# Kernel tuning notes

Measured on AMD Instinct MI355X. Metric: run time of the kernel, lower is better.

The kernel has to match this reference:

```python
import jax, jax.numpy as jnp
import numpy as np

N, T, DM = 8192, 32, 128   # nodes, patches, d_model (d_in = T*DM = 4096)
M, NNZ = 1024, 131072      # hyperedges, incidences
EPS = 1e-5
SLOPE = 0.2


def _bn(x, g, b, axes):
    # BatchNorm with batch statistics (training-mode math, eval dropout)
    m = jnp.mean(x, axis=axes, keepdims=True)
    v = jnp.var(x, axis=axes, keepdims=True)
    return (x - m) / jnp.sqrt(v + EPS) * g + b


def _hconv(x, he_attr, he_n, he_e, W, att, bias, heads):
    # PyG HypergraphConv, use_attention=True, attention_mode='node', concat=False
    out = W.shape[1] // heads
    xt = (x @ W).reshape(N, heads, out)          # [N, H, F]
    et = (he_attr @ W).reshape(M, heads, out)    # [M, H, F]
    xi = xt[he_n]                                # [nnz, H, F] gather node feats
    ej = et[he_e]                                # [nnz, H, F] gather edge feats
    alpha = jnp.sum(jnp.concatenate([xi, ej], axis=-1) * att, axis=-1)  # [nnz, H]
    alpha = jax.nn.leaky_relu(alpha, SLOPE)
    # segment softmax grouped by hyperedge (attention_mode='node')
    amax = jax.ops.segment_max(alpha, he_e, num_segments=M)
    ex = jnp.exp(alpha - amax[he_e])
    alpha = ex / jax.ops.segment_sum(ex, he_e, num_segments=M)[he_e]
    # degree normalizers (hyperedge_weight == 1)
    ones = jnp.ones((NNZ,), x.dtype)
    Dn = jax.ops.segment_sum(ones, he_n, num_segments=N)
    Dinv = jnp.where(Dn > 0, 1.0 / Dn, 0.0)
    Bm = jax.ops.segment_sum(ones, he_e, num_segments=M)
    Binv = jnp.where(Bm > 0, 1.0 / Bm, 0.0)
    # node -> edge, then edge -> node message passing
    eo = jax.ops.segment_sum(alpha[:, :, None] * Binv[he_e][:, None, None] * xi,
                             he_e, num_segments=M)                     # [M, H, F]
    no = jax.ops.segment_sum(alpha[:, :, None] * Dinv[he_n][:, None, None] * eo[he_e],
                             he_n, num_segments=N)                     # [N, H, F]
    return no.mean(axis=1) + bias  # concat=False -> mean over heads


def setup_inputs() -> dict:
    key = jax.random.key(0)
    ks = jax.random.split(key, 16)
    d_in = T * DM
    s = 0.02
    inp = {
        "x": jax.random.normal(ks[0], (N, T, DM), jnp.float32),
        "he_nodes": jax.random.randint(ks[1], (NNZ,), 0, N),
        "he_edges": jax.random.randint(ks[2], (NNZ,), 0, M),
        "W1": jax.random.normal(ks[3], (d_in, DM), jnp.float32) * s,
        "b1": jnp.zeros((DM,), jnp.float32),
        "g1": jnp.ones((DM,), jnp.float32), "be1": jnp.zeros((DM,), jnp.float32),
        "Wh1": jax.random.normal(ks[4], (DM, 4 * DM), jnp.float32) * s,
        "att1": jax.random.normal(ks[5], (1, 4, 2 * DM), jnp.float32) * s,
        "bh1": jnp.zeros((DM,), jnp.float32),
        "g2": jnp.ones((DM,), jnp.float32), "be2": jnp.zeros((DM,), jnp.float32),
        "Wh2": jax.random.normal(ks[6], (DM, DM), jnp.float32) * s,
        "att2": jax.random.normal(ks[7], (1, 1, 2 * DM), jnp.float32) * s,
        "bh2": jnp.zeros((DM,), jnp.float32),
        "g3": jnp.ones((DM,), jnp.float32), "be3": jnp.zeros((DM,), jnp.float32),
        "W3": jax.random.normal(ks[8], (DM, d_in), jnp.float32) * s,
        "b3": jnp.zeros((d_in,), jnp.float32),
        "g4": jnp.ones((DM,), jnp.float32), "be4": jnp.zeros((DM,), jnp.float32),
    }
    return inp


def reference(x, he_nodes, he_edges, W1, b1, g1, be1, Wh1, att1, bh1,
              g2, be2, Wh2, att2, bh2, g3, be3, W3, b3, g4, be4):
    src = x
    h = x.reshape(N, T * DM)
    h = jax.nn.leaky_relu(h @ W1 + b1, SLOPE)
    h = _bn(h, g1, be1, 0)
    # hyperedge_attr = incidence^T @ h  (== to_dense_adj(...).T @ h)
    he_attr = jax.ops.segment_sum(h[he_nodes], he_edges, num_segments=M)
    h = h + _hconv(h, he_attr, he_nodes, he_edges, Wh1, att1, bh1, 4)
    h = _bn(h, g2, be2, 0)
    he_attr = jax.ops.segment_sum(h[he_nodes], he_edges, num_segments=M)
    h = h + _hconv(h, he_attr, he_nodes, he_edges, Wh2, att2, bh2, 1)
    h = _bn(h, g3, be3, 0)
    h = jax.nn.leaky_relu(h @ W3 + b3, SLOPE)
    h = src + h.reshape(N, T, DM)
    h = _bn(h, g4, be4, (0, 1))  # BN over channel DM, stats over (N, T)
    return h
```

## Files before the change

kernel.cpp:

```cpp
#include <hip/hip_runtime.h>
#include <hip/hip_bf16.h>
#include <math.h>

#define NN   8192
#define TT   32
#define DIN  4096
#define MME  1024
#define NNZK 131072
#define EPSV 1e-5f
#define MALL (NN + MME)

typedef __attribute__((ext_vector_type(8))) short bf16x8;
typedef __attribute__((ext_vector_type(4))) float f32x4;

__device__ __forceinline__ float lrelu(float v){ return v > 0.f ? v : 0.2f*v; }
__device__ __forceinline__ short f2b(float f){
    union { __hip_bfloat16 h; short s; } u; u.h = __float2bfloat16(f); return u.s;
}
__device__ __forceinline__ float b2f(short s){
    union { float f; unsigned u; } u; u.u = ((unsigned)(unsigned short)s) << 16; return u.f;
}

__global__ void zero_i(int* p, int n){ int i = blockIdx.x*256 + threadIdx.x; if (i < n) p[i] = 0; }
__global__ void zero_f(float* p, int n){ int i = blockIdx.x*256 + threadIdx.x; if (i < n) p[i] = 0.f; }
__global__ void copy_i(const int* a, int* b, int n){ int i = blockIdx.x*256 + threadIdx.x; if (i < n) b[i] = a[i]; }

__global__ void count_seg(const int* __restrict__ he_n, const int* __restrict__ he_e,
                          int* __restrict__ ncnt, int* __restrict__ ecnt){
    int k = blockIdx.x*256 + threadIdx.x;
    if (k < NNZK){ atomicAdd(&ecnt[he_e[k]], 1); atomicAdd(&ncnt[he_n[k]], 1); }
}

__global__ void scan_excl(const int* __restrict__ cnt, int* __restrict__ off, int n){
    int t = threadIdx.x;
    int lane = t & 63, wv = t >> 6;
    int chunk = n >> 10;
    int base = t*chunk;
    int s = 0;
#pragma unroll 4
    for (int i = 0; i < chunk; i++) s += cnt[base+i];
    int v = s;
    for (int d = 1; d < 64; d <<= 1){
        int u = __shfl_up(v, d);
        if (lane >= d) v += u;
    }
    __shared__ int wsum[16];
    if (lane == 63) wsum[wv] = v;
    __syncthreads();
    if (wv == 0 && lane < 16){
        int w2 = wsum[lane];
        for (int d = 1; d < 16; d <<= 1){
            int u = __shfl_up(w2, d);
            if (lane >= d) w2 += u;
        }
        wsum[lane] = w2;
    }
    __syncthreads();
    int excl = v - s + (wv > 0 ? wsum[wv-1] : 0);
    for (int i = 0; i < chunk; i++){
        off[base+i] = excl;
        excl += cnt[base+i];
    }
    if (t == 1023) off[n] = excl;
}

__global__ void fill_perm(const int* __restrict__ seg, int* __restrict__ cur, int* __restrict__ perm){
    int k = blockIdx.x*256 + threadIdx.x;
    if (k < NNZK){ int p = atomicAdd(&cur[seg[k]], 1); perm[p] = k; }
}

__global__ __launch_bounds__(256) void convert_x(const float4* __restrict__ x,
                                                 bf16x8* __restrict__ xb, int n8){
    int stride = gridDim.x*256;
    for (int i = blockIdx.x*256 + threadIdx.x; i < n8; i += stride){
        float4 lo = x[2*i], hi = x[2*i+1];
        bf16x8 v;
        v[0]=f2b(lo.x); v[1]=f2b(lo.y); v[2]=f2b(lo.z); v[3]=f2b(lo.w);
        v[4]=f2b(hi.x); v[5]=f2b(hi.y); v[6]=f2b(hi.z); v[7]=f2b(hi.w);
        xb[i] = v;
    }
}

__global__ void wconv_t(const float* __restrict__ W, __hip_bfloat16* __restrict__ BT, int K, int N){
    __shared__ float tile[32][33];
    int k0 = blockIdx.y*32, n0 = blockIdx.x*32;
    int tx = threadIdx.x & 31, ty = threadIdx.x >> 5;
    for (int i = ty; i < 32; i += 8) tile[i][tx] = W[(size_t)(k0+i)*N + n0+tx];
    __syncthreads();
    for (int i = ty; i < 32; i += 8)
        BT[(size_t)(n0+i)*K + k0 + tx] = __float2bfloat16(tile[tx][i]);
}

#define SWZ(b) ((b) ^ ((((b) >> 6) & 7) << 4))

__global__ __launch_bounds__(256) void gemm_bb(
    const __hip_bfloat16* __restrict__ Ab, const __hip_bfloat16* __restrict__ Bwt,
    __hip_bfloat16* __restrict__ Cb, int M, int N, int K, int kchunk)
{
    __shared__ f32x4 WsRaw[512];
    __shared__ f32x4 XsRaw[512];
    char* Ws = (char*)WsRaw;
    char* Xs = (char*)XsRaw;
    const int tid = threadIdx.x;
    const int lane = tid & 63;
    const int w = tid >> 6;
    const int m0 = blockIdx.y << 7, n0 = blockIdx.x << 7;
    const int kz = blockIdx.z * kchunk;
    const int wN = (w >> 1) << 6, wM = (w & 1) << 6;

    const int s0 = tid, s1 = tid + 256;
    const int r0 = s0 >> 2, k0b = (s0 & 3) << 3;
    const int r1 = s1 >> 2, k1b = (s1 & 3) << 3;
    const __hip_bfloat16* pA0 = Ab + (size_t)(m0 + r0)*K + kz + k0b;
    const __hip_bfloat16* pA1 = Ab + (size_t)(m0 + r1)*K + kz + k1b;
    const __hip_bfloat16* pW0 = Bwt + (size_t)(n0 + r0)*K + kz + k0b;
    const __hip_bfloat16* pW1 = Bwt + (size_t)(n0 + r1)*K + kz + k1b;
    const int wo0 = SWZ(s0 << 4), wo1 = SWZ(s1 << 4);

    int rwOff[4], rxOff[4];
#pragma unroll
    for (int f = 0; f < 4; f++){
        rwOff[f] = SWZ((wN + f*16 + (lane & 15))*64 + ((lane >> 4) << 4));
        rxOff[f] = SWZ((wM + f*16 + (lane & 15))*64 + ((lane >> 4) << 4));
    }

    f32x4 acc[4][4] = {};

    bf16x8 a0 = *(const bf16x8*)pA0, a1 = *(const bf16x8*)pA1;
    bf16x8 w0 = *(const bf16x8*)pW0, w1 = *(const bf16x8*)pW1;

    const int nsteps = kchunk >> 5;
    for (int ks = 0; ks < nsteps; ks++){
        __syncthreads();
        *(bf16x8*)(Xs + wo0) = a0;
        *(bf16x8*)(Xs + wo1) = a1;
        *(bf16x8*)(Ws + wo0) = w0;
        *(bf16x8*)(Ws + wo1) = w1;
        __syncthreads();
        if (ks + 1 < nsteps){
            pA0 += 32; pA1 += 32; pW0 += 32; pW1 += 32;
            a0 = *(const bf16x8*)pA0; a1 = *(const bf16x8*)pA1;
            w0 = *(const bf16x8*)pW0; w1 = *(const bf16x8*)pW1;
        }
        bf16x8 wf[4], xf[4];
#pragma unroll
        for (int f = 0; f < 4; f++){
            wf[f] = *(const bf16x8*)(Ws + rwOff[f]);
            xf[f] = *(const bf16x8*)(Xs + rxOff[f]);
        }
#pragma unroll
        for (int i = 0; i < 4; i++)
#pragma unroll
            for (int j = 0; j < 4; j++)
                acc[i][j] = __builtin_amdgcn_mfma_f32_16x16x32_bf16(wf[i], xf[j], acc[i][j], 0, 0, 0);
    }

    const int mc = wM + (lane & 15);
    const int ncb = wN + ((lane >> 4) << 2);
    __hip_bfloat16* Cz = Cb + (size_t)blockIdx.z * ((size_t)M * (size_t)N);
#pragma unroll
    for (int j = 0; j < 4; j++){
        int row = m0 + mc + j*16;
#pragma unroll
        for (int i = 0; i < 4; i++){
            int col = n0 + ncb + i*16;
            f32x4 v = acc[i][j];
            short4 sv = { f2b(v[0]), f2b(v[1]), f2b(v[2]), f2b(v[3]) };
            *(short4*)&Cz[(size_t)row*N + col] = sv;
        }
    }
}

template<int MODE>
__global__ __launch_bounds__(256) void gemm_nt(
    const float* __restrict__ Aact, const __hip_bfloat16* __restrict__ Bwt,
    float* __restrict__ C, __hip_bfloat16* __restrict__ Cb, const float* __restrict__ bias,
    int M, int N, int K, int kchunk)
{
    __shared__ f32x4 WsRaw[512];
    __shared__ f32x4 XsRaw[512];
    char* Ws = (char*)WsRaw;
    char* Xs = (char*)XsRaw;
    const int tid = threadIdx.x;
    const int lane = tid & 63;
    const int w = tid >> 6;
    const int m0 = blockIdx.y << 7, n0 = blockIdx.x << 7;
    const int wN = (w >> 1) << 6, wM = (w & 1) << 6;

    const int s0 = tid, s1 = tid + 256;
    const int r0 = s0 >> 2, k0b = (s0 & 3) << 3;
    const int r1 = s1 >> 2, k1b = (s1 & 3) << 3;
    const float* pX0 = Aact + (size_t)(m0 + r0)*K + k0b;
    const float* pX1 = Aact + (size_t)(m0 + r1)*K + k1b;
    const __hip_bfloat16* pW0 = Bwt + (size_t)(n0 + r0)*K + k0b;
    const __hip_bfloat16* pW1 = Bwt + (size_t)(n0 + r1)*K + k1b;
    const int wo0 = SWZ(s0 << 4), wo1 = SWZ(s1 << 4);

    int rwOff[4], rxOff[4];
#pragma unroll
    for (int f = 0; f < 4; f++){
        rwOff[f] = SWZ((wN + f*16 + (lane & 15))*64 + ((lane >> 4) << 4));
        rxOff[f] = SWZ((wM + f*16 + (lane & 15))*64 + ((lane >> 4) << 4));
    }

    f32x4 acc[4][4] = {};

    float4 x0l = *(const float4*)pX0, x0h = *(const float4*)(pX0+4);
    float4 x1l = *(const float4*)pX1, x1h = *(const float4*)(pX1+4);
    bf16x8 w0 = *(const bf16x8*)pW0, w1 = *(const bf16x8*)pW1;

    const int nsteps = kchunk >> 5;
    for (int ks = 0; ks < nsteps; ks++){
        bf16x8 vx0, vx1;
        vx0[0]=f2b(x0l.x); vx0[1]=f2b(x0l.y); vx0[2]=f2b(x0l.z); vx0[3]=f2b(x0l.w);
        vx0[4]=f2b(x0h.x); vx0[5]=f2b(x0h.y); vx0[6]=f2b(x0h.z); vx0[7]=f2b(x0h.w);
        vx1[0]=f2b(x1l.x); vx1[1]=f2b(x1l.y); vx1[2]=f2b(x1l.z); vx1[3]=f2b(x1l.w);
        vx1[4]=f2b(x1h.x); vx1[5]=f2b(x1h.y); vx1[6]=f2b(x1h.z); vx1[7]=f2b(x1h.w);
        __syncthreads();
        *(bf16x8*)(Xs + wo0) = vx0;
        *(bf16x8*)(Xs + wo1) = vx1;
        *(bf16x8*)(Ws + wo0) = w0;
        *(bf16x8*)(Ws + wo1) = w1;
        __syncthreads();
        if (ks + 1 < nsteps){
            pX0 += 32; pX1 += 32; pW0 += 32; pW1 += 32;
            x0l = *(const float4*)pX0; x0h = *(const float4*)(pX0+4);
            x1l = *(const float4*)pX1; x1h = *(const float4*)(pX1+4);
            w0 = *(const bf16x8*)pW0;  w1 = *(const bf16x8*)pW1;
        }
        bf16x8 wf[4], xf[4];
#pragma unroll
        for (int f = 0; f < 4; f++){
            wf[f] = *(const bf16x8*)(Ws + rwOff[f]);
            xf[f] = *(const bf16x8*)(Xs + rxOff[f]);
        }
#pragma unroll
        for (int i = 0; i < 4; i++)
#pragma unroll
            for (int j = 0; j < 4; j++)
                acc[i][j] = __builtin_amdgcn_mfma_f32_16x16x32_bf16(wf[i], xf[j], acc[i][j], 0, 0, 0);
    }

    const int mc = wM + (lane & 15);
    const int ncb = wN + ((lane >> 4) << 2);
#pragma unroll
    for (int j = 0; j < 4; j++){
        int row = m0 + mc + j*16;
#pragma unroll
        for (int i = 0; i < 4; i++){
            int col = n0 + ncb + i*16;
            f32x4 v = acc[i][j];
            if (MODE == 0){
                *(float4*)&C[(size_t)row*N + col] = *(float4*)&v;
            } else if (MODE == 5){
                short4 sv = { f2b(v[0]), f2b(v[1]), f2b(v[2]), f2b(v[3]) };
                *(short4*)&Cb[(size_t)row*N + col] = sv;
            } else {
                float4 b4 = *(const float4*)&bias[col];
                short4 sv = { f2b(lrelu(v[0] + b4.x)), f2b(lrelu(v[1] + b4.y)),
                              f2b(lrelu(v[2] + b4.z)), f2b(lrelu(v[3] + b4.w)) };
                *(short4*)&Cb[(size_t)row*N + col] = sv;
            }
        }
    }
}

__global__ void reduce8s(const __hip_bfloat16* __restrict__ part, const float* __restrict__ bias,
                         float* __restrict__ out, int nf4, int parts, float* __restrict__ slots){
    int tid = threadIdx.x;
    int i = blockIdx.x*256 + tid;
    const short4* p4 = (const short4*)part;
    short4 v0 = p4[i];
    float4 s = { b2f(v0.x), b2f(v0.y), b2f(v0.z), b2f(v0.w) };
    for (int z = 1; z < parts; z++){
        short4 p = p4[(size_t)z*nf4 + i];
        s.x += b2f(p.x); s.y += b2f(p.y); s.z += b2f(p.z); s.w += b2f(p.w);
    }
    int c0 = (i & 31) << 2;
    s.x = lrelu(s.x + bias[c0+0]); s.y = lrelu(s.y + bias[c0+1]);
    s.z = lrelu(s.z + bias[c0+2]); s.w = lrelu(s.w + bias[c0+3]);
    ((float4*)out)[i] = s;
    __shared__ float S[128], Q[128];
    if (tid < 128){ S[tid] = 0.f; Q[tid] = 0.f; }
    __syncthreads();
    atomicAdd(&S[c0+0], s.x); atomicAdd(&Q[c0+0], s.x*s.x);
    atomicAdd(&S[c0+1], s.y); atomicAdd(&Q[c0+1], s.y*s.y);
    atomicAdd(&S[c0+2], s.z); atomicAdd(&Q[c0+2], s.z*s.z);
    atomicAdd(&S[c0+3], s.w); atomicAdd(&Q[c0+3], s.w*s.w);
    __syncthreads();
    if (tid < 128){
        int slot = blockIdx.x & 31;
        atomicAdd(&slots[slot*256 + tid], S[tid]);
        atomicAdd(&slots[slot*256 + 128 + tid], Q[tid]);
    }
}

__global__ __launch_bounds__(256) void final_stats(
    const bf16x8* __restrict__ xb, const bf16x8* __restrict__ f,
    float* __restrict__ slots, int n8)
{
    int tid = threadIdx.x;
    float s[8] = {0,0,0,0,0,0,0,0}, q[8] = {0,0,0,0,0,0,0,0};
    int stride = gridDim.x*256;
    for (int i = blockIdx.x*256 + tid; i < n8; i += stride){
        bf16x8 xv = xb[i], fv = f[i];
#pragma unroll
        for (int j = 0; j < 8; j++){
            float y = b2f(xv[j]) + b2f(fv[j]);
            s[j] += y; q[j] += y*y;
        }
    }
    __shared__ float S[128], Q[128];
    if (tid < 128){ S[tid] = 0.f; Q[tid] = 0.f; }
    __syncthreads();
    int c0 = (tid & 15) << 3;
#pragma unroll
    for (int j = 0; j < 8; j++){
        atomicAdd(&S[c0+j], s[j]);
        atomicAdd(&Q[c0+j], q[j]);
    }
    __syncthreads();
    if (tid < 128){
        int slot = blockIdx.x & 31;
        atomicAdd(&slots[slot*256 + tid], S[tid]);
        atomicAdd(&slots[slot*256 + 128 + tid], Q[tid]);
    }
}

__global__ __launch_bounds__(256) void final_apply(
    const bf16x8* __restrict__ xb, const bf16x8* __restrict__ f,
    const float* __restrict__ coef, float4* __restrict__ out, int n8)
{
    int tid = threadIdx.x;
    int c0 = (tid & 15) << 3;
    float sc[8], sh[8];
#pragma unroll
    for (int j = 0; j < 8; j++){ sc[j] = coef[c0+j]; sh[j] = coef[128+c0+j]; }
    int stride = gridDim.x*256;
    for (int i = blockIdx.x*256 + tid; i < n8; i += stride){
        bf16x8 xv = xb[i], fv = f[i];
        float4 lo, hi;
        lo.x = (b2f(xv[0]) + b2f(fv[0]))*sc[0] + sh[0];
        lo.y = (b2f(xv[1]) + b2f(fv[1]))*sc[1] + sh[1];
        lo.z = (b2f(xv[2]) + b2f(fv[2]))*sc[2] + sh[2];
        lo.w = (b2f(xv[3]) + b2f(fv[3]))*sc[3] + sh[3];
        hi.x = (b2f(xv[4]) + b2f(fv[4]))*sc[4] + sh[4];
        hi.y = (b2f(xv[5]) + b2f(fv[5]))*sc[5] + sh[5];
        hi.z = (b2f(xv[6]) + b2f(fv[6]))*sc[6] + sh[6];
        hi.w = (b2f(xv[7]) + b2f(fv[7]))*sc[7] + sh[7];
        out[2*i]   = lo;
        out[2*i+1] = hi;
    }
}

__global__ void bn_stats_v2(const float* __restrict__ x, float* __restrict__ slots, int rows){
    int cg = threadIdx.x & 31, rg = threadIdx.x >> 5;
    float4 s = {0,0,0,0}, q = {0,0,0,0};
    for (int r = blockIdx.x*8 + rg; r < rows; r += gridDim.x*8){
        float4 v = ((const float4*)x)[(size_t)r*32 + cg];
        s.x += v.x; q.x += v.x*v.x;
        s.y += v.y; q.y += v.y*v.y;
        s.z += v.z; q.z += v.z*v.z;
        s.w += v.w; q.w += v.w*v.w;
    }
    __shared__ float S[128], Q[128];
    if (threadIdx.x < 128){ S[threadIdx.x] = 0.f; Q[threadIdx.x] = 0.f; }
    __syncthreads();
    int c0 = cg << 2;
    atomicAdd(&S[c0+0], s.x); atomicAdd(&Q[c0+0], q.x);
    atomicAdd(&S[c0+1], s.y); atomicAdd(&Q[c0+1], q.y);
    atomicAdd(&S[c0+2], s.z); atomicAdd(&Q[c0+2], q.z);
    atomicAdd(&S[c0+3], s.w); atomicAdd(&Q[c0+3], q.w);
    __syncthreads();
    if (threadIdx.x < 128){
        int slot = blockIdx.x & 31;
        atomicAdd(&slots[slot*256 + threadIdx.x], S[threadIdx.x]);
        atomicAdd(&slots[slot*256 + 128 + threadIdx.x], Q[threadIdx.x]);
    }
}

__global__ void bn_finalize2(const float* __restrict__ slots, int nslots,
                             const float* __restrict__ g, const float* __restrict__ b,
                             float invR, float* __restrict__ coef){
    int c = threadIdx.x;
    float s = 0.f, q = 0.f;
    for (int k = 0; k < nslots; k++){ s += slots[k*256 + c]; q += slots[k*256 + 128 + c]; }
    float m = s*invR;
    float v = q*invR - m*m;
    float sc = g[c]*rsqrtf(v + EPSV);
    coef[c] = sc;
    coef[128 + c] = b[c] - m*sc;
}

__global__ void bn_apply4(float4* __restrict__ x, const float* __restrict__ coef, size_t n4){
    size_t i = (size_t)blockIdx.x*blockDim.x + threadIdx.x;
    size_t stride = (size_t)gridDim.x*blockDim.x;
    for (; i < n4; i += stride){
        int c0 = (int)(i & 31) * 4;
        float4 v = x[i];
        v.x = v.x*coef[c0+0] + coef[128+c0+0];
        v.y = v.y*coef[c0+1] + coef[128+c0+1];
        v.z = v.z*coef[c0+2] + coef[128+c0+2];
        v.w = v.w*coef[c0+3] + coef[128+c0+3];
        x[i] = v;
    }
}

__global__ void seg_sum_edge(const int* __restrict__ eoff, const int* __restrict__ eperm,
                             const int* __restrict__ he_n, const float* __restrict__ h,
                             float* __restrict__ out){
    int m = blockIdx.x, c = threadIdx.x;
    int s0 = eoff[m], cnt = eoff[m+1] - s0;
    __shared__ int sn[128];
    float acc = 0.f;
    for (int base = 0; base < cnt; base += 128){
        int i = base + c;
        if (i < cnt) sn[c] = he_n[eperm[s0+i]];
        __syncthreads();
        int lim = min(128, cnt - base);
        for (int j = 0; j < lim; j++) acc += h[(size_t)sn[j]*128 + c];
        __syncthreads();
    }
    out[(size_t)m*128 + c] = acc;
}

__global__ void row_att4b(const __hip_bfloat16* __restrict__ xt, const float* __restrict__ att,
                          int aoff, float* __restrict__ out){
    int n = blockIdx.x, lane = threadIdx.x;
#pragma unroll
    for (int h = 0; h < 4; h++){
        const __hip_bfloat16* xr = xt + (size_t)n*512 + h*128;
        const float* ar = att + h*256 + aoff;
        float s = b2f(((const short*)xr)[2*lane])*ar[2*lane]
                + b2f(((const short*)xr)[2*lane+1])*ar[2*lane+1];
        for (int d = 32; d > 0; d >>= 1) s += __shfl_down(s, d);
        if (lane == 0) out[n*4 + h] = s;
    }
}

template<int H>
__global__ void row_att(const float* __restrict__ xt, const float* __restrict__ att,
                        int aoff, float* __restrict__ out){
    int n = blockIdx.x, lane = threadIdx.x;
#pragma unroll
    for (int h = 0; h < H; h++){
        const float* xr = xt + (size_t)n*(H*128) + h*128;
        const float* ar = att + h*256 + aoff;
        float s = xr[lane]*ar[lane] + xr[lane+64]*ar[lane+64];
        for (int d = 32; d > 0; d >>= 1) s += __shfl_down(s, d);
        if (lane == 0) out[n*H + h] = s;
    }
}

template<int H>
__global__ void seg_softmax(const int* __restrict__ eoff, const int* __restrict__ eperm,
                            const int* __restrict__ he_n,
                            const float* __restrict__ ax, const float* __restrict__ ae,
                            float* __restrict__ alpha){
    int m = blockIdx.x, t = threadIdx.x;
    int s0 = eoff[m], cnt = eoff[m+1] - s0;
    if (cnt == 0) return;
    __shared__ float red[128];
    float aeh[H];
#pragma unroll
    for (int h = 0; h < H; h++) aeh[h] = ae[m*H + h];
    float lmax[H];
#pragma unroll
    for (int h = 0; h < H; h++) lmax[h] = -1e30f;
    for (int i = t; i < cnt; i += 128){
        int k = eperm[s0+i]; int n = he_n[k];
#pragma unroll
        for (int h = 0; h < H; h++){
            float v = lrelu(ax[n*H + h] + aeh[h]);
            alpha[(size_t)k*H + h] = v;
            lmax[h] = fmaxf(lmax[h], v);
        }
    }
    float gmax[H];
#pragma unroll
    for (int h = 0; h < H; h++){
        red[t] = lmax[h]; __syncthreads();
        for (int s = 64; s > 0; s >>= 1){ if (t < s) red[t] = fmaxf(red[t], red[t+s]); __syncthreads(); }
        gmax[h] = red[0]; __syncthreads();
    }
    float lsum[H];
#pragma unroll
    for (int h = 0; h < H; h++) lsum[h] = 0.f;
    for (int i = t; i < cnt; i += 128){
        int k = eperm[s0+i];
#pragma unroll
        for (int h = 0; h < H; h++){
            float ex = __expf(alpha[(size_t)k*H + h] - gmax[h]);
            alpha[(size_t)k*H + h] = ex;
            lsum[h] += ex;
        }
    }
    float ginv[H];
#pragma unroll
    for (int h = 0; h < H; h++){
        red[t] = lsum[h]; __syncthreads();
        for (int s = 64; s > 0; s >>= 1){ if (t < s) red[t] += red[t+s]; __syncthreads(); }
        ginv[h] = 1.f/red[0]; __syncthreads();
    }
    for (int i = t; i < cnt; i += 128){
        int k = eperm[s0+i];
#pragma unroll
        for (int h = 0; h < H; h++) alpha[(size_t)k*H + h] *= ginv[h];
    }
}

__global__ void seg_eo4(const int* __restrict__ eoff, const int* __restrict__ eperm,
                        const int* __restrict__ he_n,
                        const float* __restrict__ alpha, const __hip_bfloat16* __restrict__ xt,
                        float* __restrict__ eo){
    int m = blockIdx.x;
    int c = threadIdx.x & 127, hb = threadIdx.x >> 7;
    int s0 = eoff[m], cnt = eoff[m+1] - s0;
    __shared__ int sn[128];
    __shared__ float sa[128][4];
    float acc0 = 0.f, acc1 = 0.f;
    for (int base = 0; base < cnt; base += 128){
        int i = base + threadIdx.x;
        if (threadIdx.x < 128 && i < cnt){
            int k = eperm[s0+i];
            sn[threadIdx.x] = he_n[k];
#pragma unroll
            for (int h = 0; h < 4; h++) sa[threadIdx.x][h] = alpha[(size_t)k*4 + h];
        }
        __syncthreads();
        int lim = min(128, cnt - base);
        for (int j = 0; j < lim; j++){
            const short* xr = (const short*)(xt + (size_t)sn[j]*512);
            acc0 += sa[j][hb]   * b2f(xr[hb*128 + c]);
            acc1 += sa[j][hb+2] * b2f(xr[(hb+2)*128 + c]);
        }
        __syncthreads();
    }
    float binv = cnt > 0 ? 1.f/(float)cnt : 0.f;
    eo[(size_t)m*512 + hb*128 + c]     = acc0*binv;
    eo[(size_t)m*512 + (hb+2)*128 + c] = acc1*binv;
}

__global__ void seg_eo1(const int* __restrict__ eoff, const int* __restrict__ eperm,
                        const int* __restrict__ he_n,
                        const float* __restrict__ alpha, const float* __restrict__ xt,
                        float* __restrict__ eo){
    int m = blockIdx.x, c = threadIdx.x;
    int s0 = eoff[m], cnt = eoff[m+1] - s0;
    __shared__ int sn[128];
    __shared__ float sa[128];
    float acc = 0.f;
    for (int base = 0; base < cnt; base += 128){
        int i = base + c;
        if (i < cnt){
            int k = eperm[s0+i];
            sn[c] = he_n[k];
            sa[c] = alpha[k];
        }
        __syncthreads();
        int lim = min(128, cnt - base);
        for (int j = 0; j < lim; j++) acc += sa[j]*xt[(size_t)sn[j]*128 + c];
        __syncthreads();
    }
    float binv = cnt > 0 ? 1.f/(float)cnt : 0.f;
    eo[(size_t)m*128 + c] = acc*binv;
}

template<int H>
__global__ void seg_node_out(const int* __restrict__ noff, const int* __restrict__ nperm,
                             const int* __restrict__ he_e,
                             const float* __restrict__ alpha, const float* __restrict__ eo,
                             const float* __restrict__ hin, const float* __restrict__ bias,
                             float* __restrict__ hout){
    int n = blockIdx.x, c = threadIdx.x;
    int s0 = noff[n], cnt = noff[n+1] - s0;
    float acc = 0.f;
    for (int i = 0; i < cnt; i++){
        int k = nperm[s0+i]; int e = he_e[k];
        const float* er = eo + (size_t)e*(128*H);
#pragma unroll
        for (int h = 0; h < H; h++) acc += alpha[(size_t)k*H + h]*er[h*128 + c];
    }
    float dinv = cnt > 0 ? 1.f/((float)cnt*(float)H) : 0.f;
    hout[(size_t)n*128 + c] = hin[(size_t)n*128 + c] + bias[c] + acc*dinv;
}

extern "C" void kernel_launch(void* const* d_in, const int* in_sizes, int n_in,
                              void* d_out, int out_size, void* d_ws, size_t ws_size,
                              hipStream_t stream){
    const float* x    = (const float*)d_in[0];
    const int*   he_n = (const int*)  d_in[1];
    const int*   he_e = (const int*)  d_in[2];
    const float* W1   = (const float*)d_in[3];
    const float* b1   = (const float*)d_in[4];
    const float* g1   = (const float*)d_in[5];
    const float* be1  = (const float*)d_in[6];
    const float* Wh1  = (const float*)d_in[7];
    const float* att1 = (const float*)d_in[8];
    const float* bh1  = (const float*)d_in[9];
    const float* g2   = (const float*)d_in[10];
    const float* be2  = (const float*)d_in[11];
    const float* Wh2  = (const float*)d_in[12];
    const float* att2 = (const float*)d_in[13];
    const float* bh2  = (const float*)d_in[14];
    const float* g3   = (const float*)d_in[15];
    const float* be3  = (const float*)d_in[16];
    const float* W3   = (const float*)d_in[17];
    const float* b3   = (const float*)d_in[18];
    const float* g4   = (const float*)d_in[19];
    const float* be4  = (const float*)d_in[20];
    float* out = (float*)d_out;

    char* ws = (char*)d_ws;
    size_t off = 0;
    auto alloc = [&](size_t bytes)->char*{ char* p = ws + off; off += (bytes + 255) & ~(size_t)255; return p; };

    char* big = alloc((size_t)NN*DIN*2);
    __hip_bfloat16* fbuf = (__hip_bfloat16*)big;
    __hip_bfloat16* part = (__hip_bfloat16*)big;
    __hip_bfloat16* xt1b = (__hip_bfloat16*)(big + (size_t)16*NN*128*2);
    __hip_bfloat16* xbuf = (__hip_bfloat16*)alloc((size_t)NN*DIN*2);

    float* hall1  = (float*)alloc((size_t)MALL*128*4);
    float* hall2  = (float*)alloc((size_t)MALL*128*4);
    float* h3     = (float*)alloc((size_t)NN*128*4);
    float* xt2    = (float*)alloc((size_t)MALL*128*4);
    float* eo     = (float*)alloc((size_t)MME*512*4);
    float* alpha  = (float*)alloc((size_t)NNZK*4*4);
    float* ax     = (float*)alloc((size_t)NN*4*4);
    float* ae     = (float*)alloc((size_t)MME*4*4);
    float* slots  = (float*)alloc((size_t)32*256*4);
    float* coef   = (float*)alloc(256*4);
    __hip_bfloat16* W1T  = (__hip_bfloat16*)alloc((size_t)128*DIN*2);
    __hip_bfloat16* Wh1T = (__hip_bfloat16*)alloc((size_t)512*128*2);
    __hip_bfloat16* Wh2T = (__hip_bfloat16*)alloc((size_t)128*128*2);
    __hip_bfloat16* W3T  = (__hip_bfloat16*)alloc((size_t)DIN*128*2);
    int* ecnt  = (int*)alloc(MME*4);
    int* ncnt  = (int*)alloc(NN*4);
    int* eoffb = (int*)alloc((MME+1)*4);
    int* ecur  = (int*)alloc(MME*4);
    int* noffb = (int*)alloc((NN+1)*4);
    int* ncur  = (int*)alloc(NN*4);
    int* eperm = (int*)alloc((size_t)NNZK*4);
    int* nperm = (int*)alloc((size_t)NNZK*4);

    convert_x<<<2048, 256, 0, stream>>>((const float4*)x, (bf16x8*)xbuf, NN*DIN/8);

    zero_i<<<(MME+NN+255)/256, 256, 0, stream>>>(ecnt, MME+NN);
    count_seg<<<NNZK/256, 256, 0, stream>>>(he_n, he_e, ncnt, ecnt);
    scan_excl<<<1, 1024, 0, stream>>>(ecnt, eoffb, MME);
    scan_excl<<<1, 1024, 0, stream>>>(ncnt, noffb, NN);
    copy_i<<<(MME+255)/256, 256, 0, stream>>>(eoffb, ecur, MME);
    copy_i<<<(NN+255)/256, 256, 0, stream>>>(noffb, ncur, NN);
    fill_perm<<<NNZK/256, 256, 0, stream>>>(he_e, ecur, eperm);
    fill_perm<<<NNZK/256, 256, 0, stream>>>(he_n, ncur, nperm);

    wconv_t<<<dim3(128/32, DIN/32), 256, 0, stream>>>(W1,  W1T,  DIN, 128);
    wconv_t<<<dim3(512/32, 128/32), 256, 0, stream>>>(Wh1, Wh1T, 128, 512);
    wconv_t<<<dim3(128/32, 128/32), 256, 0, stream>>>(Wh2, Wh2T, 128, 128);
    wconv_t<<<dim3(DIN/32, 128/32), 256, 0, stream>>>(W3,  W3T,  128, DIN);

    gemm_bb<<<dim3(1, NN/128, 16), 256, 0, stream>>>(xbuf, W1T, part, NN, 128, DIN, DIN/16);
    zero_f<<<32, 256, 0, stream>>>(slots, 32*256);
    reduce8s<<<NN*128/4/256, 256, 0, stream>>>(part, b1, hall1, NN*128/4, 16, slots);
    bn_finalize2<<<1, 128, 0, stream>>>(slots, 32, g1, be1, 1.f/NN, coef);
    bn_apply4<<<1024, 256, 0, stream>>>((float4*)hall1, coef, (size_t)NN*32);

    seg_sum_edge<<<MME, 128, 0, stream>>>(eoffb, eperm, he_n, hall1, hall1 + (size_t)NN*128);
    gemm_nt<5><<<dim3(512/128, MALL/128, 1), 256, 0, stream>>>(hall1, Wh1T, nullptr, xt1b, nullptr, MALL, 512, 128, 128);
    row_att4b<<<NN, 64, 0, stream>>>(xt1b, att1, 0, ax);
    row_att4b<<<MME, 64, 0, stream>>>(xt1b + (size_t)NN*512, att1, 128, ae);
    seg_softmax<4><<<MME, 128, 0, stream>>>(eoffb, eperm, he_n, ax, ae, alpha);
    seg_eo4<<<MME, 256, 0, stream>>>(eoffb, eperm, he_n, alpha, xt1b, eo);
    seg_node_out<4><<<NN, 128, 0, stream>>>(noffb, nperm, he_e, alpha, eo, hall1, bh1, hall2);
    zero_f<<<32, 256, 0, stream>>>(slots, 32*256);
    bn_stats_v2<<<256, 256, 0, stream>>>(hall2, slots, NN);
    bn_finalize2<<<1, 128, 0, stream>>>(slots, 32, g2, be2, 1.f/NN, coef);
    bn_apply4<<<1024, 256, 0, stream>>>((float4*)hall2, coef, (size_t)NN*32);

    seg_sum_edge<<<MME, 128, 0, stream>>>(eoffb, eperm, he_n, hall2, hall2 + (size_t)NN*128);
    gemm_nt<0><<<dim3(1, MALL/128, 1), 256, 0, stream>>>(hall2, Wh2T, xt2, nullptr, nullptr, MALL, 128, 128, 128);
    row_att<1><<<NN, 64, 0, stream>>>(xt2, att2, 0, ax);
    row_att<1><<<MME, 64, 0, stream>>>(xt2 + (size_t)NN*128, att2, 128, ae);
    seg_softmax<1><<<MME, 128, 0, stream>>>(eoffb, eperm, he_n, ax, ae, alpha);
    seg_eo1<<<MME, 128, 0, stream>>>(eoffb, eperm, he_n, alpha, xt2, eo);
    seg_node_out<1><<<NN, 128, 0, stream>>>(noffb, nperm, he_e, alpha, eo, hall2, bh2, h3);
    zero_f<<<32, 256, 0, stream>>>(slots, 32*256);
    bn_stats_v2<<<256, 256, 0, stream>>>(h3, slots, NN);
    bn_finalize2<<<1, 128, 0, stream>>>(slots, 32, g3, be3, 1.f/NN, coef);
    bn_apply4<<<1024, 256, 0, stream>>>((float4*)h3, coef, (size_t)NN*32);

    gemm_nt<3><<<dim3(DIN/128, NN/128, 1), 256, 0, stream>>>(h3, W3T, nullptr, fbuf, b3, NN, DIN, 128, 128);
    zero_f<<<32, 256, 0, stream>>>(slots, 32*256);
    final_stats<<<2048, 256, 0, stream>>>((const bf16x8*)xbuf, (const bf16x8*)fbuf, slots, NN*DIN/8);
    bn_finalize2<<<1, 128, 0, stream>>>(slots, 32, g4, be4, 1.f/((float)NN*TT), coef);
    final_apply<<<2048, 256, 0, stream>>>((const bf16x8*)xbuf, (const bf16x8*)fbuf, coef, (float4*)out, NN*DIN/8);
}
```

Baseline: 556.8 us.

## Fuse BN apply into final GEMM, store sorted neighbor ids, use bf16 layer-2 features

Folds the third BatchNorm's scale and shift into the A-operand load of the final GEMM, which removes a separate pass over h3. The scan now also initialises the cursor arrays, so the copy kernels are gone. The permutation fill records node and edge ids in sorted order so later segment kernels skip a level of indirection. Layer-2 transformed features are stored in bf16, the seg_eo kernels read two values per load with more unrolling, and the stats slot count drops from 32 to 8. Fewer slots means more atomic contention per slot, and bf16 storage of xt2 lowers precision.

```diff
diff --git a/kernel.cpp b/kernel.cpp
--- a/kernel.cpp
+++ b/kernel.cpp
@@ -9,6 +9,7 @@
 #define NNZK 131072
 #define EPSV 1e-5f
 #define MALL (NN + MME)
+#define NSLOT 8
 
 typedef __attribute__((ext_vector_type(8))) short bf16x8;
 typedef __attribute__((ext_vector_type(4))) float f32x4;
@@ -23,7 +24,6 @@
 
 __global__ void zero_i(int* p, int n){ int i = blockIdx.x*256 + threadIdx.x; if (i < n) p[i] = 0; }
 __global__ void zero_f(float* p, int n){ int i = blockIdx.x*256 + threadIdx.x; if (i < n) p[i] = 0.f; }
-__global__ void copy_i(const int* a, int* b, int n){ int i = blockIdx.x*256 + threadIdx.x; if (i < n) b[i] = a[i]; }
 
 __global__ void count_seg(const int* __restrict__ he_n, const int* __restrict__ he_e,
                           int* __restrict__ ncnt, int* __restrict__ ecnt){
@@ -31,7 +31,8 @@
     if (k < NNZK){ atomicAdd(&ecnt[he_e[k]], 1); atomicAdd(&ncnt[he_n[k]], 1); }
 }
 
-__global__ void scan_excl(const int* __restrict__ cnt, int* __restrict__ off, int n){
+__global__ void scan_excl(const int* __restrict__ cnt, int* __restrict__ off,
+                          int* __restrict__ cur, int n){
     int t = threadIdx.x;
     int lane = t & 63, wv = t >> 6;
     int chunk = n >> 10;
@@ -59,14 +60,20 @@
     int excl = v - s + (wv > 0 ? wsum[wv-1] : 0);
     for (int i = 0; i < chunk; i++){
         off[base+i] = excl;
+        cur[base+i] = excl;
         excl += cnt[base+i];
     }
     if (t == 1023) off[n] = excl;
 }
 
-__global__ void fill_perm(const int* __restrict__ seg, int* __restrict__ cur, int* __restrict__ perm){
+__global__ void fill_perm2(const int* __restrict__ seg, const int* __restrict__ other,
+                           int* __restrict__ cur, int* __restrict__ perm, int* __restrict__ oth){
     int k = blockIdx.x*256 + threadIdx.x;
-    if (k < NNZK){ int p = atomicAdd(&cur[seg[k]], 1); perm[p] = k; }
+    if (k < NNZK){
+        int p = atomicAdd(&cur[seg[k]], 1);
+        perm[p] = k;
+        oth[p] = other[k];
+    }
 }
 
 __global__ __launch_bounds__(256) void convert_x(const float4* __restrict__ x,
@@ -174,8 +181,8 @@
 template<int MODE>
 __global__ __launch_bounds__(256) void gemm_nt(
     const float* __restrict__ Aact, const __hip_bfloat16* __restrict__ Bwt,
-    float* __restrict__ C, __hip_bfloat16* __restrict__ Cb, const float* __restrict__ bias,
-    int M, int N, int K, int kchunk)
+    __hip_bfloat16* __restrict__ Cb, const float* __restrict__ bias,
+    const float* __restrict__ coefA, int M, int N, int K, int kchunk)
 {
     __shared__ f32x4 WsRaw[512];
     __shared__ f32x4 XsRaw[512];
@@ -211,6 +218,21 @@
 
     const int nsteps = kchunk >> 5;
     for (int ks = 0; ks < nsteps; ks++){
+        if (MODE == 7){
+            int kc0 = k0b + ks*32, kc1 = k1b + ks*32;
+            float4 s0v = *(const float4*)&coefA[kc0],     s0w = *(const float4*)&coefA[kc0+4];
+            float4 h0v = *(const float4*)&coefA[128+kc0], h0w = *(const float4*)&coefA[128+kc0+4];
+            float4 s1v = *(const float4*)&coefA[kc1],     s1w = *(const float4*)&coefA[kc1+4];
+            float4 h1v = *(const float4*)&coefA[128+kc1], h1w = *(const float4*)&coefA[128+kc1+4];
+            x0l.x = x0l.x*s0v.x + h0v.x; x0l.y = x0l.y*s0v.y + h0v.y;
+            x0l.z = x0l.z*s0v.z + h0v.z; x0l.w = x0l.w*s0v.w + h0v.w;
+            x0h.x = x0h.x*s0w.x + h0w.x; x0h.y = x0h.y*s0w.y + h0w.y;
+            x0h.z = x0h.z*s0w.z + h0w.z; x0h.w = x0h.w*s0w.w + h0w.w;
+            x1l.x = x1l.x*s1v.x + h1v.x; x1l.y = x1l.y*s1v.y + h1v.y;
+            x1l.z = x1l.z*s1v.z + h1v.z; x1l.w = x1l.w*s1v.w + h1v.w;
+            x1h.x = x1h.x*s1w.x + h1w.x; x1h.y = x1h.y*s1w.y + h1w.y;
+            x1h.z = x1h.z*s1w.z + h1w.z; x1h.w = x1h.w*s1w.w + h1w.w;
+        }
         bf16x8 vx0, vx1;
         vx0[0]=f2b(x0l.x); vx0[1]=f2b(x0l.y); vx0[2]=f2b(x0l.z); vx0[3]=f2b(x0l.w);
         vx0[4]=f2b(x0h.x); vx0[5]=f2b(x0h.y); vx0[6]=f2b(x0h.z); vx0[7]=f2b(x0h.w);
@@ -250,15 +272,13 @@
         for (int i = 0; i < 4; i++){
             int col = n0 + ncb + i*16;
             f32x4 v = acc[i][j];
-            if (MODE == 0){
-                *(float4*)&C[(size_t)row*N + col] = *(float4*)&v;
-            } else if (MODE == 5){
-                short4 sv = { f2b(v[0]), f2b(v[1]), f2b(v[2]), f2b(v[3]) };
-                *(short4*)&Cb[(size_t)row*N + col] = sv;
-            } else {
+            if (MODE == 7){
                 float4 b4 = *(const float4*)&bias[col];
                 short4 sv = { f2b(lrelu(v[0] + b4.x)), f2b(lrelu(v[1] + b4.y)),
                               f2b(lrelu(v[2] + b4.z)), f2b(lrelu(v[3] + b4.w)) };
+                *(short4*)&Cb[(size_t)row*N + col] = sv;
+            } else {
+                short4 sv = { f2b(v[0]), f2b(v[1]), f2b(v[2]), f2b(v[3]) };
                 *(short4*)&Cb[(size_t)row*N + col] = sv;
             }
         }
@@ -289,7 +309,7 @@
     atomicAdd(&S[c0+3], s.w); atomicAdd(&Q[c0+3], s.w*s.w);
     __syncthreads();
     if (tid < 128){
-        int slot = blockIdx.x & 31;
+        int slot = blockIdx.x & (NSLOT-1);
         atomicAdd(&slots[slot*256 + tid], S[tid]);
         atomicAdd(&slots[slot*256 + 128 + tid], Q[tid]);
     }
@@ -321,7 +341,7 @@
     }
     __syncthreads();
     if (tid < 128){
-        int slot = blockIdx.x & 31;
+        int slot = blockIdx.x & (NSLOT-1);
         atomicAdd(&slots[slot*256 + tid], S[tid]);
         atomicAdd(&slots[slot*256 + 128 + tid], Q[tid]);
     }
@@ -373,7 +393,7 @@
     atomicAdd(&S[c0+3], s.w); atomicAdd(&Q[c0+3], q.w);
     __syncthreads();
     if (threadIdx.x < 128){
-        int slot = blockIdx.x & 31;
+        int slot = blockIdx.x & (NSLOT-1);
         atomicAdd(&slots[slot*256 + threadIdx.x], S[threadIdx.x]);
         atomicAdd(&slots[slot*256 + 128 + threadIdx.x], Q[threadIdx.x]);
     }
@@ -406,16 +426,15 @@
     }
 }
 
-__global__ void seg_sum_edge(const int* __restrict__ eoff, const int* __restrict__ eperm,
-                             const int* __restrict__ he_n, const float* __restrict__ h,
-                             float* __restrict__ out){
+__global__ void seg_sum_edge(const int* __restrict__ eoff, const int* __restrict__ enode,
+                             const float* __restrict__ h, float* __restrict__ out){
     int m = blockIdx.x, c = threadIdx.x;
     int s0 = eoff[m], cnt = eoff[m+1] - s0;
     __shared__ int sn[128];
     float acc = 0.f;
     for (int base = 0; base < cnt; base += 128){
         int i = base + c;
-        if (i < cnt) sn[c] = he_n[eperm[s0+i]];
+        if (i < cnt) sn[c] = enode[s0+i];
         __syncthreads();
         int lim = min(128, cnt - base);
         for (int j = 0; j < lim; j++) acc += h[(size_t)sn[j]*128 + c];
@@ -429,32 +448,29 @@
     int n = blockIdx.x, lane = threadIdx.x;
 #pragma unroll
     for (int h = 0; h < 4; h++){
-        const __hip_bfloat16* xr = xt + (size_t)n*512 + h*128;
+        const short* xr = (const short*)(xt + (size_t)n*512 + h*128);
         const float* ar = att + h*256 + aoff;
-        float s = b2f(((const short*)xr)[2*lane])*ar[2*lane]
-                + b2f(((const short*)xr)[2*lane+1])*ar[2*lane+1];
+        unsigned u = *(const unsigned*)(xr + 2*lane);
+        float s = b2f((short)(u & 0xffff))*ar[2*lane] + b2f((short)(u >> 16))*ar[2*lane+1];
         for (int d = 32; d > 0; d >>= 1) s += __shfl_down(s, d);
         if (lane == 0) out[n*4 + h] = s;
     }
 }
 
-template<int H>
-__global__ void row_att(const float* __restrict__ xt, const float* __restrict__ att,
-                        int aoff, float* __restrict__ out){
+__global__ void row_att1b(const __hip_bfloat16* __restrict__ xt, const float* __restrict__ att,
+                          int aoff, float* __restrict__ out){
     int n = blockIdx.x, lane = threadIdx.x;
-#pragma unroll
-    for (int h = 0; h < H; h++){
-        const float* xr = xt + (size_t)n*(H*128) + h*128;
-        const float* ar = att + h*256 + aoff;
-        float s = xr[lane]*ar[lane] + xr[lane+64]*ar[lane+64];
-        for (int d = 32; d > 0; d >>= 1) s += __shfl_down(s, d);
-        if (lane == 0) out[n*H + h] = s;
-    }
+    const short* xr = (const short*)(xt + (size_t)n*128);
+    const float* ar = att + aoff;
+    unsigned u = *(const unsigned*)(xr + 2*lane);
+    float s = b2f((short)(u & 0xffff))*ar[2*lane] + b2f((short)(u >> 16))*ar[2*lane+1];
+    for (int d = 32; d > 0; d >>= 1) s += __shfl_down(s, d);
+    if (lane == 0) out[n] = s;
 }
 
 template<int H>
 __global__ void seg_softmax(const int* __restrict__ eoff, const int* __restrict__ eperm,
-                            const int* __restrict__ he_n,
+                            const int* __restrict__ enode,
                             const float* __restrict__ ax, const float* __restrict__ ae,
                             float* __restrict__ alpha){
     int m = blockIdx.x, t = threadIdx.x;
@@ -468,7 +484,7 @@
 #pragma unroll
     for (int h = 0; h < H; h++) lmax[h] = -1e30f;
     for (int i = t; i < cnt; i += 128){
-        int k = eperm[s0+i]; int n = he_n[k];
+        int k = eperm[s0+i]; int n = enode[s0+i];
 #pragma unroll
         for (int h = 0; h < H; h++){
             float v = lrelu(ax[n*H + h] + aeh[h]);
@@ -510,41 +526,44 @@
 }
 
 __global__ void seg_eo4(const int* __restrict__ eoff, const int* __restrict__ eperm,
-                        const int* __restrict__ he_n,
+                        const int* __restrict__ enode,
                         const float* __restrict__ alpha, const __hip_bfloat16* __restrict__ xt,
                         float* __restrict__ eo){
     int m = blockIdx.x;
-    int c = threadIdx.x & 127, hb = threadIdx.x >> 7;
+    int t = threadIdx.x;
+    int h = t >> 6, c2 = t & 63;
     int s0 = eoff[m], cnt = eoff[m+1] - s0;
     __shared__ int sn[128];
     __shared__ float sa[128][4];
     float acc0 = 0.f, acc1 = 0.f;
     for (int base = 0; base < cnt; base += 128){
-        int i = base + threadIdx.x;
-        if (threadIdx.x < 128 && i < cnt){
+        int i = base + t;
+        if (t < 128 && i < cnt){
             int k = eperm[s0+i];
-            sn[threadIdx.x] = he_n[k];
-#pragma unroll
-            for (int h = 0; h < 4; h++) sa[threadIdx.x][h] = alpha[(size_t)k*4 + h];
+            sn[t] = enode[s0+i];
+#pragma unroll
+            for (int hh = 0; hh < 4; hh++) sa[t][hh] = alpha[(size_t)k*4 + hh];
         }
         __syncthreads();
         int lim = min(128, cnt - base);
+#pragma unroll 4
         for (int j = 0; j < lim; j++){
-            const short* xr = (const short*)(xt + (size_t)sn[j]*512);
-            acc0 += sa[j][hb]   * b2f(xr[hb*128 + c]);
-            acc1 += sa[j][hb+2] * b2f(xr[(hb+2)*128 + c]);
+            unsigned u = *(const unsigned*)((const short*)xt + (size_t)sn[j]*512 + h*128 + 2*c2);
+            float a = sa[j][h];
+            acc0 += a * b2f((short)(u & 0xffff));
+            acc1 += a * b2f((short)(u >> 16));
         }
         __syncthreads();
     }
     float binv = cnt > 0 ? 1.f/(float)cnt : 0.f;
-    eo[(size_t)m*512 + hb*128 + c]     = acc0*binv;
-    eo[(size_t)m*512 + (hb+2)*128 + c] = acc1*binv;
-}
-
-__global__ void seg_eo1(const int* __restrict__ eoff, const int* __restrict__ eperm,
-                        const int* __restrict__ he_n,
-                        const float* __restrict__ alpha, const float* __restrict__ xt,
-                        float* __restrict__ eo){
+    float2 st = { acc0*binv, acc1*binv };
+    *(float2*)&eo[(size_t)m*512 + h*128 + 2*c2] = st;
+}
+
+__global__ void seg_eo1b(const int* __restrict__ eoff, const int* __restrict__ eperm,
+                         const int* __restrict__ enode,
+                         const float* __restrict__ alpha, const __hip_bfloat16* __restrict__ xt,
+                         float* __restrict__ eo){
     int m = blockIdx.x, c = threadIdx.x;
     int s0 = eoff[m], cnt = eoff[m+1] - s0;
     __shared__ int sn[128];
@@ -553,13 +572,14 @@
     for (int base = 0; base < cnt; base += 128){
         int i = base + c;
         if (i < cnt){
-            int k = eperm[s0+i];
-            sn[c] = he_n[k];
-            sa[c] = alpha[k];
+            sn[c] = enode[s0+i];
+            sa[c] = alpha[eperm[s0+i]];
         }
         __syncthreads();
         int lim = min(128, cnt - base);
-        for (int j = 0; j < lim; j++) acc += sa[j]*xt[(size_t)sn[j]*128 + c];
+#pragma unroll 4
+        for (int j = 0; j < lim; j++)
+            acc += sa[j]*b2f(((const short*)xt)[(size_t)sn[j]*128 + c]);
         __syncthreads();
     }
     float binv = cnt > 0 ? 1.f/(float)cnt : 0.f;
@@ -568,7 +588,7 @@
 
 template<int H>
 __global__ void seg_node_out(const int* __restrict__ noff, const int* __restrict__ nperm,
-                             const int* __restrict__ he_e,
+                             const int* __restrict__ nedge,
                              const float* __restrict__ alpha, const float* __restrict__ eo,
                              const float* __restrict__ hin, const float* __restrict__ bias,
                              float* __restrict__ hout){
@@ -576,7 +596,7 @@
     int s0 = noff[n], cnt = noff[n+1] - s0;
     float acc = 0.f;
     for (int i = 0; i < cnt; i++){
-        int k = nperm[s0+i]; int e = he_e[k];
+        int k = nperm[s0+i]; int e = nedge[s0+i];
         const float* er = eo + (size_t)e*(128*H);
 #pragma unroll
         for (int h = 0; h < H; h++) acc += alpha[(size_t)k*H + h]*er[h*128 + c];
@@ -624,12 +644,12 @@
     float* hall1  = (float*)alloc((size_t)MALL*128*4);
     float* hall2  = (float*)alloc((size_t)MALL*128*4);
     float* h3     = (float*)alloc((size_t)NN*128*4);
-    float* xt2    = (float*)alloc((size_t)MALL*128*4);
+    __hip_bfloat16* xt2b = (__hip_bfloat16*)alloc((size_t)MALL*128*2);
     float* eo     = (float*)alloc((size_t)MME*512*4);
     float* alpha  = (float*)alloc((size_t)NNZK*4*4);
     float* ax     = (float*)alloc((size_t)NN*4*4);
     float* ae     = (float*)alloc((size_t)MME*4*4);
-    float* slots  = (float*)alloc((size_t)32*256*4);
+    float* slots  = (float*)alloc((size_t)NSLOT*256*4);
     float* coef   = (float*)alloc(256*4);
     __hip_bfloat16* W1T  = (__hip_bfloat16*)alloc((size_t)128*DIN*2);
     __hip_bfloat16* Wh1T = (__hip_bfloat16*)alloc((size_t)512*128*2);
@@ -643,17 +663,17 @@
     int* ncur  = (int*)alloc(NN*4);
     int* eperm = (int*)alloc((size_t)NNZK*4);
     int* nperm = (int*)alloc((size_t)NNZK*4);
+    int* enode = (int*)alloc((size_t)NNZK*4);
+    int* nedge = (int*)alloc((size_t)NNZK*4);
 
     convert_x<<<2048, 256, 0, stream>>>((const float4*)x, (bf16x8*)xbuf, NN*DIN/8);
 
     zero_i<<<(MME+NN+255)/256, 256, 0, stream>>>(ecnt, MME+NN);
     count_seg<<<NNZK/256, 256, 0, stream>>>(he_n, he_e, ncnt, ecnt);
-    scan_excl<<<1, 1024, 0, stream>>>(ecnt, eoffb, MME);
-    scan_excl<<<1, 1024, 0, stream>>>(ncnt, noffb, NN);
-    copy_i<<<(MME+255)/256, 256, 0, stream>>>(eoffb, ecur, MME);
-    copy_i<<<(NN+255)/256, 256, 0, stream>>>(noffb, ncur, NN);
-    fill_perm<<<NNZK/256, 256, 0, stream>>>(he_e, ecur, eperm);
-    fill_perm<<<NNZK/256, 256, 0, stream>>>(he_n, ncur, nperm);
+    scan_excl<<<1, 1024, 0, stream>>>(ecnt, eoffb, ecur, MME);
+    scan_excl<<<1, 1024, 0, stream>>>(ncnt, noffb, ncur, NN);
+    fill_perm2<<<NNZK/256, 256, 0, stream>>>(he_e, he_n, ecur, eperm, enode);
+    fill_perm2<<<NNZK/256, 256, 0, stream>>>(he_n, he_e, ncur, nperm, nedge);
 
     wconv_t<<<dim3(128/32, DIN/32), 256, 0, stream>>>(W1,  W1T,  DIN, 128);
     wconv_t<<<dim3(512/32, 128/32), 256, 0, stream>>>(Wh1, Wh1T, 128, 512);
@@ -661,38 +681,38 @@
     wconv_t<<<dim3(DIN/32, 128/32), 256, 0, stream>>>(W3,  W3T,  128, DIN);
 
     gemm_bb<<<dim3(1, NN/128, 16), 256, 0, stream>>>(xbuf, W1T, part, NN, 128, DIN, DIN/16);
-    zero_f<<<32, 256, 0, stream>>>(slots, 32*256);
+    zero_f<<<NSLOT, 256, 0, stream>>>(slots, NSLOT*256);
     reduce8s<<<NN*128/4/256, 256, 0, stream>>>(part, b1, hall1, NN*128/4, 16, slots);
-    bn_finalize2<<<1, 128, 0, stream>>>(slots, 32, g1, be1, 1.f/NN, coef);
+    bn_finalize2<<<1, 128, 0, stream>>>(slots, NSLOT, g1, be1, 1.f/NN, coef);
     bn_apply4<<<1024, 256, 0, stream>>>((float4*)hall1, coef, (size_t)NN*32);
 
-    seg_sum_edge<<<MME, 128, 0, stream>>>(eoffb, eperm, he_n, hall1, hall1 + (size_t)NN*128);
-    gemm_nt<5><<<dim3(512/128, MALL/128, 1), 256, 0, stream>>>(hall1, Wh1T, nullptr, xt1b, nullptr, MALL, 512, 128, 128);
+    seg_sum_edge<<<MME, 128, 0, stream>>>(eoffb, enode, hall1, hall1 + (size_t)NN*128);
+    gemm_nt<5><<<dim3(512/128, MALL/128, 1), 256, 0, stream>>>(hall1, Wh1T, xt1b, nullptr, nullptr, MALL, 512, 128, 128);
     row_att4b<<<NN, 64, 0, stream>>>(xt1b, att1, 0, ax);
     row_att4b<<<MME, 64, 0, stream>>>(xt1b + (size_t)NN*512, att1, 128, ae);
-    seg_softmax<4><<<MME, 128, 0, stream>>>(eoffb, eperm, he_n, ax, ae, alpha);
-    seg_eo4<<<MME, 256, 0, stream>>>(eoffb, eperm, he_n, alpha, xt1b, eo);
-    seg_node_out<4><<<NN, 128, 0, stream>>>(noffb, nperm, he_e, alpha, eo, hall1, bh1, hall2);
-    zero_f<<<32, 256, 0, stream>>>(slots, 32*256);
+    seg_softmax<4><<<MME, 128, 0, stream>>>(eoffb, eperm, enode, ax, ae, alpha);
+    seg_eo4<<<MME, 256, 0, stream>>>(eoffb, eperm, enode, alpha, xt1b, eo);
+    seg_node_out<4><<<NN, 128, 0, stream>>>(noffb, nperm, nedge, alpha, eo, hall1, bh1, hall2);
+    zero_f<<<NSLOT, 256, 0, stream>>>(slots, NSLOT*256);
     bn_stats_v2<<<256, 256, 0, stream>>>(hall2, slots, NN);
-    bn_finalize2<<<1, 128, 0, stream>>>(slots, 32, g2, be2, 1.f/NN, coef);
+    bn_finalize2<<<1, 128, 0, stream>>>(slots, NSLOT, g2, be2, 1.f/NN, coef);
     bn_apply4<<<1024, 256, 0, stream>>>((float4*)hall2, coef, (size_t)NN*32);
 
-    seg_sum_edge<<<MME, 128, 0, stream>>>(eoffb, eperm, he_n, hall2, hall2 + (size_t)NN*128);
-    gemm_nt<0><<<dim3(1, MALL/128, 1), 256, 0, stream>>>(hall2, Wh2T, xt2, nullptr, nullptr, MALL, 128, 128, 128);
-    row_att<1><<<NN, 64, 0, stream>>>(xt2, att2, 0, ax);
-    row_att<1><<<MME, 64, 0, stream>>>(xt2 + (size_t)NN*128, att2, 128, ae);
-    seg_softmax<1><<<MME, 128, 0, stream>>>(eoffb, eperm, he_n, ax, ae, alpha);
-    seg_eo1<<<MME, 128, 0, stream>>>(eoffb, eperm, he_n, alpha, xt2, eo);
-    seg_node_out<1><<<NN, 128, 0, stream>>>(noffb, nperm, he_e, alpha, eo, hall2, bh2, h3);
-    zero_f<<<32, 256, 0, stream>>>(slots, 32*256);
+    seg_sum_edge<<<MME, 128, 0, stream>>>(eoffb, enode, hall2, hall2 + (size_t)NN*128);
+    gemm_nt<5><<<dim3(1, MALL/128, 1), 256, 0, stream>>>(hall2, Wh2T, xt2b, nullptr, nullptr, MALL, 128, 128, 128);
+    row_att1b<<<NN, 64, 0, stream>>>(xt2b, att2, 0, ax);
+    row_att1b<<<MME, 64, 0, stream>>>(xt2b + (size_t)NN*128, att2, 128, ae);
+    seg_softmax<1><<<MME, 128, 0, stream>>>(eoffb, eperm, enode, ax, ae, alpha);
+    seg_eo1b<<<MME, 128, 0, stream>>>(eoffb, eperm, enode, alpha, xt2b, eo);
+    seg_node_out<1><<<NN, 128, 0, stream>>>(noffb, nperm, nedge, alpha, eo, hall2, bh2, h3);
+
+    zero_f<<<NSLOT, 256, 0, stream>>>(slots, NSLOT*256);
     bn_stats_v2<<<256, 256, 0, stream>>>(h3, slots, NN);
-    bn_finalize2<<<1, 128, 0, stream>>>(slots, 32, g3, be3, 1.f/NN, coef);
-    bn_apply4<<<1024, 256, 0, stream>>>((float4*)h3, coef, (size_t)NN*32);
-
-    gemm_nt<3><<<dim3(DIN/128, NN/128, 1), 256, 0, stream>>>(h3, W3T, nullptr, fbuf, b3, NN, DIN, 128, 128);
-    zero_f<<<32, 256, 0, stream>>>(slots, 32*256);
+    bn_finalize2<<<1, 128, 0, stream>>>(slots, NSLOT, g3, be3, 1.f/NN, coef);
+
+    gemm_nt<7><<<dim3(DIN/128, NN/128, 1), 256, 0, stream>>>(h3, W3T, fbuf, b3, coef, NN, DIN, 128, 128);
+    zero_f<<<NSLOT, 256, 0, stream>>>(slots, NSLOT*256);
     final_stats<<<2048, 256, 0, stream>>>((const bf16x8*)xbuf, (const bf16x8*)fbuf, slots, NN*DIN/8);
-    bn_finalize2<<<1, 128, 0, stream>>>(slots, 32, g4, be4, 1.f/((float)NN*TT), coef);
+    bn_finalize2<<<1, 128, 0, stream>>>(slots, NSLOT, g4, be4, 1.f/((float)NN*TT), coef);
     final_apply<<<2048, 256, 0, stream>>>((const bf16x8*)xbuf, (const bf16x8*)fbuf, coef, (float4*)out, NN*DIN/8);
 }
```

After: 521.2 us. -6.4%, faster.
